# Optimization experiments

Hardware: AMD Instinct MI355X
Metric: run time of the kernel (lower is better)

The kernel has to match this reference:

```python
import jax, jax.numpy as jnp
import numpy as np

B, S, E = 4, 4096, 1024
H = 16
D = E // H  # head_dim = 64


def setup_inputs() -> dict:
    key = jax.random.key(0)
    kx, kk, kq, kv = jax.random.split(key, 4)
    scale = 1.0 / np.sqrt(E)
    return {
        "x": jax.random.normal(kx, (B, S, E), dtype=jnp.float32),
        # torch nn.Linear weight shape: [out_features, in_features] = [D, E]
        "Wk": jax.random.uniform(kk, (D, E), dtype=jnp.float32, minval=-scale, maxval=scale),
        "Wq": jax.random.uniform(kq, (D, E), dtype=jnp.float32, minval=-scale, maxval=scale),
        "Wv": jax.random.uniform(kv, (D, E), dtype=jnp.float32, minval=-scale, maxval=scale),
    }


def reference(x, Wk, Wq, Wv):
    # Projections: x @ W^T  -> [B, S, D]
    k = jnp.einsum('bse,de->bsd', x, Wk)
    q = jnp.einsum('bse,de->bsd', x, Wq)
    v = jnp.einsum('bse,de->bsd', x, Wv)
    # Scaled scores [B, S, S]
    scores = jnp.einsum('bqd,bkd->bqk', q, k) * (D ** -0.5)
    # Causal mask: position q attends to k <= q
    causal = jnp.tril(jnp.ones((S, S), dtype=bool))
    scores = jnp.where(causal, scores, -jnp.inf)
    attn = jax.nn.softmax(scores, axis=-1)
    # dropout omitted (eval mode / attn_pdrop=0)
    out = jnp.einsum('bqk,bkd->bqd', attn, v)
    return out
```

## Files before the change

### kernel.cpp

```cpp
#include <hip/hip_runtime.h>
#include <hip/hip_bf16.h>
#include <stdint.h>

#define BB 4
#define SS 4096
#define EE 1024
#define DD 64

typedef __attribute__((ext_vector_type(8))) short short8;
typedef __attribute__((ext_vector_type(4))) float f32x4;

__device__ inline uint32_t cvtpk(float lo, float hi) {
    uint32_t r;
    asm("v_cvt_pk_bf16_f32 %0, %1, %2" : "=v"(r) : "v"(lo), "v"(hi));
    return r;
}
__device__ inline float bf2f_lo(uint32_t u) {
    union { uint32_t u; float f; } v; v.u = u << 16; return v.f;
}
__device__ inline float bf2f_hi(uint32_t u) {
    union { uint32_t u; float f; } v; v.u = u & 0xFFFF0000u; return v.f;
}

#define GL16(g, l) __builtin_amdgcn_global_load_lds( \
    (const __attribute__((address_space(1))) void*)(g), \
    (__attribute__((address_space(3))) void*)(l), 16, 0, 0)

__global__ __launch_bounds__(256) void wconv_kernel(
    const float* __restrict__ Wq, const float* __restrict__ Wk,
    const float* __restrict__ Wv, ushort* __restrict__ Wb)
{
    int tid = blockIdx.x * 256 + threadIdx.x;
    int sel = tid >> 13;
    int off = (tid & 8191) * 8;
    const float* src = (sel == 0) ? Wq : ((sel == 1) ? Wk : Wv);
    float4 a = *reinterpret_cast<const float4*>(src + off);
    float4 b = *reinterpret_cast<const float4*>(src + off + 4);
    uint4 o;
    o.x = cvtpk(a.x, a.y); o.y = cvtpk(a.z, a.w);
    o.z = cvtpk(b.x, b.y); o.w = cvtpk(b.z, b.w);
    *reinterpret_cast<uint4*>(Wb + (size_t)sel * 65536 + off) = o;
}

__global__ __launch_bounds__(256) void proj_kernel(
    const float* __restrict__ x, const ushort* __restrict__ Wb,
    ushort* __restrict__ q_ws, ushort* __restrict__ k_ws, ushort* __restrict__ vT_ws)
{
    __shared__ __align__(16) char smem[3 * 20480];
    const int t = threadIdx.x;
    const int wid = t >> 6, lane = t & 63, g = lane >> 4, lr = lane & 15;
    const int m0 = blockIdx.x * 64;
    const int NT = EE / 32;

    f32x4 acc[3][4];
#pragma unroll
    for (int ni = 0; ni < 3; ++ni)
#pragma unroll
        for (int mi = 0; mi < 4; ++mi) acc[ni][mi] = (f32x4)(0.0f);

#define PSTAGE(KT, BUFI) do { \
    char* xb_ = smem + (BUFI) * 20480; \
    char* wb_ = xb_ + 8192; \
    int e0_ = (KT) * 32; \
    _Pragma("unroll") \
    for (int i = 0; i < 2; ++i) { \
        int v = i * 256 + t; int row = v >> 3, c = v & 7; \
        GL16(&x[(size_t)(m0 + row) * EE + e0_ + ((c ^ (row & 7)) << 2)], xb_ + v * 16); \
    } \
    _Pragma("unroll") \
    for (int i = 0; i < 3; ++i) { \
        int v = i * 256 + t; int row = v >> 2, u = v & 3; \
        GL16(&Wb[(size_t)row * EE + e0_ + ((u ^ (row & 3)) << 3)], wb_ + v * 16); \
    } \
} while (0)

    PSTAGE(0, 0); PSTAGE(1, 1); PSTAGE(2, 2);

    for (int kt = 0; kt < NT; ++kt) {
        asm volatile("s_waitcnt vmcnt(10)" ::: "memory");
        __builtin_amdgcn_s_barrier();
        __builtin_amdgcn_sched_barrier(0);

        const char* xb = smem + (kt % 3) * 20480;
        const char* wb = xb + 8192;

        short8 af[3], bf[4];
#pragma unroll
        for (int ni = 0; ni < 3; ++ni) {
            int row = wid * 48 + ni * 16 + lr;
            af[ni] = *reinterpret_cast<const short8*>(wb + row * 64 + ((g ^ (lr & 3)) << 4));
        }
#pragma unroll
        for (int mi = 0; mi < 4; ++mi) {
            int row = mi * 16 + lr;
            int u0 = (2 * g) ^ (lr & 7);
            f32x4 lo = *reinterpret_cast<const f32x4*>(xb + row * 128 + u0 * 16);
            f32x4 hi = *reinterpret_cast<const f32x4*>(xb + row * 128 + (u0 ^ 1) * 16);
            union { short8 s; uint32_t u[4]; } p;
            p.u[0] = cvtpk(lo[0], lo[1]); p.u[1] = cvtpk(lo[2], lo[3]);
            p.u[2] = cvtpk(hi[0], hi[1]); p.u[3] = cvtpk(hi[2], hi[3]);
            bf[mi] = p.s;
        }
#pragma unroll
        for (int ni = 0; ni < 3; ++ni)
#pragma unroll
            for (int mi = 0; mi < 4; ++mi)
                acc[ni][mi] = __builtin_amdgcn_mfma_f32_16x16x32_bf16(af[ni], bf[mi], acc[ni][mi], 0, 0, 0);

        asm volatile("s_waitcnt lgkmcnt(0)" ::: "memory");
        __builtin_amdgcn_sched_barrier(0);
        __builtin_amdgcn_s_barrier();
        __builtin_amdgcn_sched_barrier(0);

        int nx = (kt + 3 < NT) ? kt + 3 : NT - 1;
        PSTAGE(nx, kt % 3);
    }

#pragma unroll
    for (int ni = 0; ni < 3; ++ni) {
        int n0 = wid * 48 + ni * 16 + 4 * g;
        int sel = n0 >> 6, d0 = n0 & 63;
#pragma unroll
        for (int mi = 0; mi < 4; ++mi) {
            int m = m0 + mi * 16 + lr;
            int b = m >> 12, s = m & (SS - 1);
            uint2 p;
            p.x = cvtpk(acc[ni][mi][0], acc[ni][mi][1]);
            p.y = cvtpk(acc[ni][mi][2], acc[ni][mi][3]);
            if (sel == 0) {
                *reinterpret_cast<uint2*>(q_ws + ((size_t)b * SS + s) * DD + d0) = p;
            } else if (sel == 1) {
                *reinterpret_cast<uint2*>(k_ws + ((size_t)b * SS + s) * DD + d0) = p;
            } else {
                vT_ws[((size_t)b * DD + d0 + 0) * SS + s] = (ushort)(p.x & 0xFFFF);
                vT_ws[((size_t)b * DD + d0 + 1) * SS + s] = (ushort)(p.x >> 16);
                vT_ws[((size_t)b * DD + d0 + 2) * SS + s] = (ushort)(p.y & 0xFFFF);
                vT_ws[((size_t)b * DD + d0 + 3) * SS + s] = (ushort)(p.y >> 16);
            }
        }
    }
}

__global__ __launch_bounds__(512) void attn_kernel(
    const ushort* __restrict__ q_ws, const ushort* __restrict__ k_ws,
    const ushort* __restrict__ vT_ws, uint32_t* __restrict__ pO32,
    float* __restrict__ pml)
{
    __shared__ __align__(16) char kv_lds[2][32768];
    const int t = threadIdx.x;
    const int wid = t >> 6, lane = t & 63, g = lane >> 4, lr = lane & 15;
    const int bid = blockIdx.x;
    const int f = bid & 3;
    const int b = (bid >> 2) & 3;
    const int qblk = 31 - (bid >> 4);
    const int qb_w = qblk * 128 + wid * 16;

    const ushort* qp = q_ws + ((size_t)b * SS + qb_w + lr) * DD;
    short8 qf0 = *reinterpret_cast<const short8*>(qp + g * 8);
    short8 qf1 = *reinterpret_cast<const short8*>(qp + 32 + g * 8);

    float l_r = 0.0f;
    f32x4 acc[4];
#pragma unroll
    for (int i = 0; i < 4; ++i) acc[i] = (f32x4)(0.0f);

    const float sc = 0.125f * 1.44269504f;
    const float MB = 5.770780164f;
    const int nt = qblk + 1;
    const int nfull = ((qb_w - 127) >> 7) + 1;
    const int cs = (nt + 3) >> 2;
    const int t0 = f * cs;
    const int t1 = min(nt, (f + 1) * cs);
    const ushort* kbase = k_ws + (size_t)b * SS * DD;
    const ushort* vbase = vT_ws + (size_t)b * DD * SS;

    const int s0 = g & 1, hi = g >> 1;
    const int idxA = ((lr + 16 * ((s0 << 1) | hi)) << 2);
    const int idxB = idxA ^ 128;

#define ASTAGE(KT, BUFI) do { \
    char* kb_ = kv_lds[BUFI]; \
    int kv0_ = (KT) * 128; \
    _Pragma("unroll") \
    for (int i = 0; i < 2; ++i) { \
        int v = i * 512 + t; int row = v >> 3, c = v & 7; \
        GL16(kbase + (size_t)(kv0_ + row) * DD + ((c ^ (row & 7)) << 3), kb_ + v * 16); \
    } \
    _Pragma("unroll") \
    for (int i = 0; i < 2; ++i) { \
        int v = i * 512 + t; int row = v >> 4, c = v & 15; \
        GL16(vbase + (size_t)row * SS + kv0_ + ((c ^ ((row & 7) << 1)) << 3), kb_ + 16384 + v * 16); \
    } \
} while (0)

    if (t0 < t1) {
        ASTAGE(t0, 0);
        ASTAGE((t0 + 1 < t1) ? t0 + 1 : t0, 1);

        for (int kt = t0; kt < t1; ++kt) {
            const int cur = (kt - t0) & 1;
            asm volatile("s_waitcnt vmcnt(4)" ::: "memory");
            __builtin_amdgcn_s_barrier();
            __builtin_amdgcn_sched_barrier(0);

            const char* kb = kv_lds[cur];
            const char* vb = kb + 16384;
            const int kv0 = kt * 128;

            f32x4 sfr[8];
            __builtin_amdgcn_s_setprio(1);
#pragma unroll
            for (int nf = 0; nf < 8; ++nf) {
                int row = nf * 16 + lr;
                short8 b0 = *reinterpret_cast<const short8*>(kb + row * 128 + ((g ^ (row & 7)) << 4));
                short8 b1 = *reinterpret_cast<const short8*>(kb + row * 128 + (((4 + g) ^ (row & 7)) << 4));
                f32x4 s_ = (f32x4)(0.0f);
                s_ = __builtin_amdgcn_mfma_f32_16x16x32_bf16(b0, qf0, s_, 0, 0, 0);
                s_ = __builtin_amdgcn_mfma_f32_16x16x32_bf16(b1, qf1, s_, 0, 0, 0);
                sfr[nf] = s_;
            }
            __builtin_amdgcn_s_setprio(0);

            if (kt >= nfull) {
#pragma unroll
                for (int nf = 0; nf < 8; ++nf)
#pragma unroll
                    for (int jr = 0; jr < 4; ++jr)
                        if (kv0 + nf * 16 + 4 * g + jr > qb_w + lr) sfr[nf][jr] = -1e30f;
            }

            float ps = 0.0f;
            uint32_t pk[16];
#pragma unroll
            for (int nf = 0; nf < 8; ++nf) {
                float e0_ = exp2f(fmaf(sfr[nf][0], sc, -MB));
                float e1_ = exp2f(fmaf(sfr[nf][1], sc, -MB));
                float e2_ = exp2f(fmaf(sfr[nf][2], sc, -MB));
                float e3_ = exp2f(fmaf(sfr[nf][3], sc, -MB));
                ps += (e0_ + e1_) + (e2_ + e3_);
                pk[nf * 2 + 0] = cvtpk(e0_, e1_);
                pk[nf * 2 + 1] = cvtpk(e2_, e3_);
            }
            l_r += ps;

            uint32_t pw[4][4];
#pragma unroll
            for (int cc = 0; cc < 4; ++cc) {
                uint32_t r0 = (uint32_t)__builtin_amdgcn_ds_permute(idxA, (int)(s0 ? pk[cc * 4 + 2] : pk[cc * 4 + 0]));
                uint32_t r1 = (uint32_t)__builtin_amdgcn_ds_permute(idxA, (int)(s0 ? pk[cc * 4 + 3] : pk[cc * 4 + 1]));
                uint32_t r2 = (uint32_t)__builtin_amdgcn_ds_permute(idxB, (int)(s0 ? pk[cc * 4 + 0] : pk[cc * 4 + 2]));
                uint32_t r3 = (uint32_t)__builtin_amdgcn_ds_permute(idxB, (int)(s0 ? pk[cc * 4 + 1] : pk[cc * 4 + 3]));
                pw[cc][0] = hi ? r2 : r0;
                pw[cc][1] = hi ? r3 : r1;
                pw[cc][2] = hi ? r0 : r2;
                pw[cc][3] = hi ? r1 : r3;
            }

            __builtin_amdgcn_s_setprio(1);
#pragma unroll
            for (int cc = 0; cc < 4; ++cc) {
                union { uint32_t u[4]; short8 s; } pb;
                pb.u[0] = pw[cc][0]; pb.u[1] = pw[cc][1];
                pb.u[2] = pw[cc][2]; pb.u[3] = pw[cc][3];
#pragma unroll
                for (int df = 0; df < 4; ++df) {
                    int row = df * 16 + lr;
                    short8 vb_ = *reinterpret_cast<const short8*>(
                        vb + row * 256 + (((cc * 4 + g) ^ ((row & 7) << 1)) << 4));
                    acc[df] = __builtin_amdgcn_mfma_f32_16x16x32_bf16(vb_, pb.s, acc[df], 0, 0, 0);
                }
            }
            __builtin_amdgcn_s_setprio(0);

            asm volatile("s_waitcnt lgkmcnt(0)" ::: "memory");
            __builtin_amdgcn_sched_barrier(0);
            __builtin_amdgcn_s_barrier();
            __builtin_amdgcn_sched_barrier(0);

            int nx = (kt + 2 < t1) ? kt + 2 : t1 - 1;
            ASTAGE(nx, cur);
        }
    }

    l_r += __shfl_xor(l_r, 16);
    l_r += __shfl_xor(l_r, 32);
    const int pidx = ((b * 256 + qblk * 8 + wid) * 4 + f);
    uint32_t* po = pO32 + (size_t)pidx * 512;
#pragma unroll
    for (int df = 0; df < 4; ++df) {
        po[(df * 8 + 2 * g + 0) * 16 + lr] = cvtpk(acc[df][0], acc[df][1]);
        po[(df * 8 + 2 * g + 1) * 16 + lr] = cvtpk(acc[df][2], acc[df][3]);
    }
    if (g == 0) pml[(size_t)pidx * 16 + lr] = l_r;
}

__global__ __launch_bounds__(64) void combine_kernel(
    const uint32_t* __restrict__ pO32, const float* __restrict__ pml,
    float* __restrict__ out)
{
    const int t = threadIdx.x;
    const int q = t & 15, dblk = t >> 4;
    const int grp = blockIdx.x;
    const int b = grp >> 8, qt = grp & 255;
    const int qb = qt * 16;

    float l = 0.0f;
#pragma unroll
    for (int f = 0; f < 4; ++f) l += pml[(size_t)(grp * 4 + f) * 16 + q];

    float o[16];
#pragma unroll
    for (int i = 0; i < 16; ++i) o[i] = 0.0f;
#pragma unroll
    for (int f = 0; f < 4; ++f) {
        const uint32_t* src = pO32 + (size_t)(grp * 4 + f) * 512 + dblk * 128 + q;
#pragma unroll
        for (int r0 = 0; r0 < 8; ++r0) {
            uint32_t u = src[r0 * 16];
            o[2 * r0 + 0] += bf2f_lo(u);
            o[2 * r0 + 1] += bf2f_hi(u);
        }
    }
    float inv = 1.0f / l;
    float* op = out + ((size_t)b * SS + qb + q) * DD + dblk * 16;
#pragma unroll
    for (int i = 0; i < 4; ++i) {
        float4 st;
        st.x = o[4 * i + 0] * inv; st.y = o[4 * i + 1] * inv;
        st.z = o[4 * i + 2] * inv; st.w = o[4 * i + 3] * inv;
        *reinterpret_cast<float4*>(op + 4 * i) = st;
    }
}

extern "C" void kernel_launch(void* const* d_in, const int* in_sizes, int n_in,
                              void* d_out, int out_size, void* d_ws, size_t ws_size,
                              hipStream_t stream) {
    const float* x  = (const float*)d_in[0];
    const float* Wk = (const float*)d_in[1];
    const float* Wq = (const float*)d_in[2];
    const float* Wv = (const float*)d_in[3];
    ushort* q_ws  = (ushort*)d_ws;
    ushort* k_ws  = q_ws + (size_t)BB * SS * DD;
    ushort* vT_ws = k_ws + (size_t)BB * SS * DD;
    ushort* Wb    = vT_ws + (size_t)BB * SS * DD;
    uint32_t* pO32 = (uint32_t*)(Wb + 192 * 1024);
    float* pml     = (float*)(pO32 + (size_t)4096 * 512);
    float* out = (float*)d_out;

    hipLaunchKernelGGL(wconv_kernel, dim3(96), dim3(256), 0, stream, Wq, Wk, Wv, Wb);
    hipLaunchKernelGGL(proj_kernel, dim3(BB * SS / 64), dim3(256), 0, stream,
                       x, Wb, q_ws, k_ws, vT_ws);
    hipLaunchKernelGGL(attn_kernel, dim3(BB * 32 * 4), dim3(512), 0, stream,
                       q_ws, k_ws, vT_ws, pO32, pml);
    hipLaunchKernelGGL(combine_kernel, dim3(BB * SS / 16), dim3(64), 0, stream,
                       pO32, pml, out);
}
```

Measured before the change: 61.36 us.

## Double-step projection K-loop with four LDS stages to halve barriers

The projection GEMM now uses four shared-memory stage buffers instead of three and handles two K-tiles between each pair of workgroup barriers. Each iteration issues prefetches for two future tiles. The aim is to halve the barrier and waitcnt synchronisation per K-tile and give the scheduler more MFMA work between syncs. In exchange it uses more LDS per block, which could reduce occupancy, and it changes how far ahead loads are issued relative to their use.

```diff
diff --git a/kernel.cpp b/kernel.cpp
--- a/kernel.cpp
+++ b/kernel.cpp
@@ -46,7 +46,7 @@
     const float* __restrict__ x, const ushort* __restrict__ Wb,
     ushort* __restrict__ q_ws, ushort* __restrict__ k_ws, ushort* __restrict__ vT_ws)
 {
-    __shared__ __align__(16) char smem[3 * 20480];
+    __shared__ __align__(16) char smem[4 * 20480];
     const int t = threadIdx.x;
     const int wid = t >> 6, lane = t & 63, g = lane >> 4, lr = lane & 15;
     const int m0 = blockIdx.x * 64;
@@ -74,46 +74,52 @@
     } \
 } while (0)
 
-    PSTAGE(0, 0); PSTAGE(1, 1); PSTAGE(2, 2);
-
-    for (int kt = 0; kt < NT; ++kt) {
+#define PCOMPUTE(BUFI) do { \
+    const char* xb = smem + (BUFI) * 20480; \
+    const char* wb = xb + 8192; \
+    short8 af[3], bf[4]; \
+    _Pragma("unroll") \
+    for (int ni = 0; ni < 3; ++ni) { \
+        int row = wid * 48 + ni * 16 + lr; \
+        af[ni] = *reinterpret_cast<const short8*>(wb + row * 64 + ((g ^ (lr & 3)) << 4)); \
+    } \
+    _Pragma("unroll") \
+    for (int mi = 0; mi < 4; ++mi) { \
+        int row = mi * 16 + lr; \
+        int u0 = (2 * g) ^ (lr & 7); \
+        f32x4 lo = *reinterpret_cast<const f32x4*>(xb + row * 128 + u0 * 16); \
+        f32x4 hi = *reinterpret_cast<const f32x4*>(xb + row * 128 + (u0 ^ 1) * 16); \
+        union { short8 s; uint32_t u[4]; } p; \
+        p.u[0] = cvtpk(lo[0], lo[1]); p.u[1] = cvtpk(lo[2], lo[3]); \
+        p.u[2] = cvtpk(hi[0], hi[1]); p.u[3] = cvtpk(hi[2], hi[3]); \
+        bf[mi] = p.s; \
+    } \
+    _Pragma("unroll") \
+    for (int ni = 0; ni < 3; ++ni) \
+        _Pragma("unroll") \
+        for (int mi = 0; mi < 4; ++mi) \
+            acc[ni][mi] = __builtin_amdgcn_mfma_f32_16x16x32_bf16(af[ni], bf[mi], acc[ni][mi], 0, 0, 0); \
+} while (0)
+
+    PSTAGE(0, 0); PSTAGE(1, 1); PSTAGE(2, 2); PSTAGE(3, 3);
+
+    for (int ss = 0; ss < NT / 2; ++ss) {
+        const int kt0 = 2 * ss, kt1 = 2 * ss + 1;
         asm volatile("s_waitcnt vmcnt(10)" ::: "memory");
         __builtin_amdgcn_s_barrier();
         __builtin_amdgcn_sched_barrier(0);
 
-        const char* xb = smem + (kt % 3) * 20480;
-        const char* wb = xb + 8192;
-
-        short8 af[3], bf[4];
-#pragma unroll
-        for (int ni = 0; ni < 3; ++ni) {
-            int row = wid * 48 + ni * 16 + lr;
-            af[ni] = *reinterpret_cast<const short8*>(wb + row * 64 + ((g ^ (lr & 3)) << 4));
-        }
-#pragma unroll
-        for (int mi = 0; mi < 4; ++mi) {
-            int row = mi * 16 + lr;
-            int u0 = (2 * g) ^ (lr & 7);
-            f32x4 lo = *reinterpret_cast<const f32x4*>(xb + row * 128 + u0 * 16);
-            f32x4 hi = *reinterpret_cast<const f32x4*>(xb + row * 128 + (u0 ^ 1) * 16);
-            union { short8 s; uint32_t u[4]; } p;
-            p.u[0] = cvtpk(lo[0], lo[1]); p.u[1] = cvtpk(lo[2], lo[3]);
-            p.u[2] = cvtpk(hi[0], hi[1]); p.u[3] = cvtpk(hi[2], hi[3]);
-            bf[mi] = p.s;
-        }
-#pragma unroll
-        for (int ni = 0; ni < 3; ++ni)
-#pragma unroll
-            for (int mi = 0; mi < 4; ++mi)
-                acc[ni][mi] = __builtin_amdgcn_mfma_f32_16x16x32_bf16(af[ni], bf[mi], acc[ni][mi], 0, 0, 0);
+        PCOMPUTE(kt0 & 3);
+        PCOMPUTE(kt1 & 3);
 
         asm volatile("s_waitcnt lgkmcnt(0)" ::: "memory");
         __builtin_amdgcn_sched_barrier(0);
         __builtin_amdgcn_s_barrier();
         __builtin_amdgcn_sched_barrier(0);
 
-        int nx = (kt + 3 < NT) ? kt + 3 : NT - 1;
-        PSTAGE(nx, kt % 3);
+        int s0_ = kt0 + 4, s1_ = kt1 + 4;
+        PSTAGE(s0_ < NT ? s0_ : NT - 1, kt0 & 3);
+        PSTAGE(s1_ < NT ? s1_ : NT - 1, kt1 & 3);
     }
 
 #pragma unroll
```

Measured after the change: 61.86 us. About the same (+0.8%).

## Split projection kernel across Q/K/V selectors to triple grid size

Applied to the files above, without the earlier changes.

The projection kernel now launches 768 blocks, one per 64-row tile and output matrix (Q, K or V), instead of 256 blocks that each computed all three. Each block stages only its 64-row slice of the bf16 weights and keeps fewer accumulators, so it uses less shared memory and fewer registers. This should raise occupancy and fill more CUs. The cost is that each x tile is loaded from global memory and converted to bf16 three times instead of once.

```diff
diff --git a/kernel.cpp b/kernel.cpp
--- a/kernel.cpp
+++ b/kernel.cpp
@@ -46,20 +46,19 @@
     const float* __restrict__ x, const ushort* __restrict__ Wb,
     ushort* __restrict__ q_ws, ushort* __restrict__ k_ws, ushort* __restrict__ vT_ws)
 {
-    __shared__ __align__(16) char smem[3 * 20480];
+    __shared__ __align__(16) char smem[3 * 12288];
     const int t = threadIdx.x;
     const int wid = t >> 6, lane = t & 63, g = lane >> 4, lr = lane & 15;
-    const int m0 = blockIdx.x * 64;
+    const int sel = blockIdx.x >> 8;
+    const int m0 = (blockIdx.x & 255) * 64;
     const int NT = EE / 32;
 
-    f32x4 acc[3][4];
-#pragma unroll
-    for (int ni = 0; ni < 3; ++ni)
-#pragma unroll
-        for (int mi = 0; mi < 4; ++mi) acc[ni][mi] = (f32x4)(0.0f);
+    f32x4 acc[4];
+#pragma unroll
+    for (int i = 0; i < 4; ++i) acc[i] = (f32x4)(0.0f);
 
 #define PSTAGE(KT, BUFI) do { \
-    char* xb_ = smem + (BUFI) * 20480; \
+    char* xb_ = smem + (BUFI) * 12288; \
     char* wb_ = xb_ + 8192; \
     int e0_ = (KT) * 32; \
     _Pragma("unroll") \
@@ -67,45 +66,42 @@
         int v = i * 256 + t; int row = v >> 3, c = v & 7; \
         GL16(&x[(size_t)(m0 + row) * EE + e0_ + ((c ^ (row & 7)) << 2)], xb_ + v * 16); \
     } \
-    _Pragma("unroll") \
-    for (int i = 0; i < 3; ++i) { \
-        int v = i * 256 + t; int row = v >> 2, u = v & 3; \
-        GL16(&Wb[(size_t)row * EE + e0_ + ((u ^ (row & 3)) << 3)], wb_ + v * 16); \
+    { \
+        int v = t; int row = v >> 2, u = v & 3; \
+        GL16(&Wb[(size_t)(sel * 64 + row) * EE + e0_ + ((u ^ (row & 3)) << 3)], wb_ + v * 16); \
     } \
 } while (0)
 
     PSTAGE(0, 0); PSTAGE(1, 1); PSTAGE(2, 2);
 
     for (int kt = 0; kt < NT; ++kt) {
-        asm volatile("s_waitcnt vmcnt(10)" ::: "memory");
+        asm volatile("s_waitcnt vmcnt(6)" ::: "memory");
         __builtin_amdgcn_s_barrier();
         __builtin_amdgcn_sched_barrier(0);
 
-        const char* xb = smem + (kt % 3) * 20480;
+        const char* xb = smem + (kt % 3) * 12288;
         const char* wb = xb + 8192;
 
-        short8 af[3], bf[4];
-#pragma unroll
-        for (int ni = 0; ni < 3; ++ni) {
-            int row = wid * 48 + ni * 16 + lr;
+        short8 af[4];
+#pragma unroll
+        for (int ni = 0; ni < 4; ++ni) {
+            int row = ni * 16 + lr;
             af[ni] = *reinterpret_cast<const short8*>(wb + row * 64 + ((g ^ (lr & 3)) << 4));
         }
-#pragma unroll
-        for (int mi = 0; mi < 4; ++mi) {
-            int row = mi * 16 + lr;
+        short8 bfr;
+        {
+            int row = wid * 16 + lr;
             int u0 = (2 * g) ^ (lr & 7);
             f32x4 lo = *reinterpret_cast<const f32x4*>(xb + row * 128 + u0 * 16);
             f32x4 hi = *reinterpret_cast<const f32x4*>(xb + row * 128 + (u0 ^ 1) * 16);
             union { short8 s; uint32_t u[4]; } p;
             p.u[0] = cvtpk(lo[0], lo[1]); p.u[1] = cvtpk(lo[2], lo[3]);
             p.u[2] = cvtpk(hi[0], hi[1]); p.u[3] = cvtpk(hi[2], hi[3]);
-            bf[mi] = p.s;
-        }
-#pragma unroll
-        for (int ni = 0; ni < 3; ++ni)
-#pragma unroll
-            for (int mi = 0; mi < 4; ++mi)
-                acc[ni][mi] = __builtin_amdgcn_mfma_f32_16x16x32_bf16(af[ni], bf[mi], acc[ni][mi], 0, 0, 0);
+            bfr = p.s;
+        }
+#pragma unroll
+        for (int ni = 0; ni < 4; ++ni)
+            acc[ni] = __builtin_amdgcn_mfma_f32_16x16x32_bf16(af[ni], bfr, acc[ni], 0, 0, 0);
 
         asm volatile("s_waitcnt lgkmcnt(0)" ::: "memory");
         __builtin_amdgcn_sched_barrier(0);
@@ -116,27 +112,23 @@
         PSTAGE(nx, kt % 3);
     }
 
-#pragma unroll
-    for (int ni = 0; ni < 3; ++ni) {
-        int n0 = wid * 48 + ni * 16 + 4 * g;
-        int sel = n0 >> 6, d0 = n0 & 63;
-#pragma unroll
-        for (int mi = 0; mi < 4; ++mi) {
-            int m = m0 + mi * 16 + lr;
-            int b = m >> 12, s = m & (SS - 1);
-            uint2 p;
-            p.x = cvtpk(acc[ni][mi][0], acc[ni][mi][1]);
-            p.y = cvtpk(acc[ni][mi][2], acc[ni][mi][3]);
-            if (sel == 0) {
-                *reinterpret_cast<uint2*>(q_ws + ((size_t)b * SS + s) * DD + d0) = p;
-            } else if (sel == 1) {
-                *reinterpret_cast<uint2*>(k_ws + ((size_t)b * SS + s) * DD + d0) = p;
-            } else {
-                vT_ws[((size_t)b * DD + d0 + 0) * SS + s] = (ushort)(p.x & 0xFFFF);
-                vT_ws[((size_t)b * DD + d0 + 1) * SS + s] = (ushort)(p.x >> 16);
-                vT_ws[((size_t)b * DD + d0 + 2) * SS + s] = (ushort)(p.y & 0xFFFF);
-                vT_ws[((size_t)b * DD + d0 + 3) * SS + s] = (ushort)(p.y >> 16);
-            }
+    const int m = m0 + wid * 16 + lr;
+    const int b = m >> 12, s = m & (SS - 1);
+#pragma unroll
+    for (int ni = 0; ni < 4; ++ni) {
+        int d0 = ni * 16 + 4 * g;
+        uint2 p;
+        p.x = cvtpk(acc[ni][0], acc[ni][1]);
+        p.y = cvtpk(acc[ni][2], acc[ni][3]);
+        if (sel == 0) {
+            *reinterpret_cast<uint2*>(q_ws + ((size_t)b * SS + s) * DD + d0) = p;
+        } else if (sel == 1) {
+            *reinterpret_cast<uint2*>(k_ws + ((size_t)b * SS + s) * DD + d0) = p;
+        } else {
+            vT_ws[((size_t)b * DD + d0 + 0) * SS + s] = (ushort)(p.x & 0xFFFF);
+            vT_ws[((size_t)b * DD + d0 + 1) * SS + s] = (ushort)(p.x >> 16);
+            vT_ws[((size_t)b * DD + d0 + 2) * SS + s] = (ushort)(p.y & 0xFFFF);
+            vT_ws[((size_t)b * DD + d0 + 3) * SS + s] = (ushort)(p.y >> 16);
         }
     }
 }
@@ -348,7 +340,7 @@
     float* out = (float*)d_out;
 
     hipLaunchKernelGGL(wconv_kernel, dim3(96), dim3(256), 0, stream, Wq, Wk, Wv, Wb);
-    hipLaunchKernelGGL(proj_kernel, dim3(BB * SS / 64), dim3(256), 0, stream,
+    hipLaunchKernelGGL(proj_kernel, dim3(768), dim3(256), 0, stream,
                        x, Wb, q_ws, k_ws, vT_ws);
     hipLaunchKernelGGL(attn_kernel, dim3(BB * 32 * 4), dim3(512), 0, stream,
                        q_ws, k_ws, vT_ws, pO32, pml);
```

After: 62.19 us. No clear change (+1.4%).
